# Optimization experiments

Measured on AMD Instinct MI355X. Metric: run time of the kernel, lower is better.

## Reference

```python
import jax, jax.numpy as jnp
import numpy as np

B, S, E = 256, 512, 768          # batch, seq_len, embed_dim (= 2*hidden_dim)
MD = 2 * 384 + 1                 # memory feature dim after location column = 769
HOPS, OUT = 3, 3


def setup_inputs() -> dict:
    key = jax.random.key(0)
    ks = jax.random.split(key, 9)
    memory = jax.random.normal(ks[0], (B, S, E), dtype=jnp.float32)
    aspect = jax.random.normal(ks[1], (B, E), dtype=jnp.float32)
    att_w = jax.random.normal(ks[2], (MD + 2 * E,), dtype=jnp.float32) * 0.02
    att_b = jnp.zeros((1,), dtype=jnp.float32)
    gru_w_ih = jax.random.normal(ks[3], (3 * E, MD), dtype=jnp.float32) * 0.02
    gru_w_hh = jax.random.normal(ks[4], (3 * E, E), dtype=jnp.float32) * 0.02
    gru_b_ih = jnp.zeros((3 * E,), dtype=jnp.float32)
    gru_b_hh = jnp.zeros((3 * E,), dtype=jnp.float32)
    dense_w = jax.random.normal(ks[5], (E, OUT), dtype=jnp.float32) * 0.02
    dense_b = jnp.zeros((OUT,), dtype=jnp.float32)
    memory_len = jax.random.randint(ks[6], (B,), S // 2, S + 1, dtype=jnp.int32)
    left_len = jax.random.randint(ks[7], (B,), 0, 64, dtype=jnp.int32)
    aspect_len = jax.random.randint(ks[8], (B,), 1, 8, dtype=jnp.int32)
    return dict(memory=memory, aspect=aspect, att_w=att_w, att_b=att_b,
                gru_w_ih=gru_w_ih, gru_w_hh=gru_w_hh, gru_b_ih=gru_b_ih,
                gru_b_hh=gru_b_hh, dense_w=dense_w, dense_b=dense_b,
                memory_len=memory_len, left_len=left_len, aspect_len=aspect_len,
                hops=HOPS)


def _locationed_memory(memory, memory_len, left_len, aspect_len):
    # Vectorized form of the nested python loop: per-position location-decay
    # weight and signed-offset column u, only for idx < memory_len.
    dt = memory.dtype
    idx = jnp.arange(memory.shape[1], dtype=jnp.int32)[None, :]   # [1,S]
    start = left_len[:, None]
    alen = aspect_len[:, None]
    mlen = memory_len[:, None]
    before = idx < start
    after_off = idx - start - alen + 1
    u = jnp.where(before, idx - start,
                  jnp.where(idx < start + alen, 0, after_off)).astype(dt)
    l = jnp.where(before, start - idx,
                  jnp.where(idx < start + alen, 0, after_off)).astype(dt)
    valid = idx < mlen
    w = jnp.where(valid, 1.0 - l / mlen.astype(dt), 1.0)
    u = jnp.where(valid, u, 0.0)
    mem = memory * w[:, :, None]
    return jnp.concatenate([mem, u[:, :, None]], axis=-1)        # [B,S,MD]


def _gru_cell(x, h, w_ih, w_hh, b_ih, b_hh):
    gi = x @ w_ih.T + b_ih
    gh = h @ w_hh.T + b_hh
    ir, iz, in_ = jnp.split(gi, 3, axis=-1)
    hr, hz, hn = jnp.split(gh, 3, axis=-1)
    r = jax.nn.sigmoid(ir + hr)
    z = jax.nn.sigmoid(iz + hz)
    n = jnp.tanh(in_ + r * hn)
    return (1.0 - z) * n + z * h


def reference(memory, aspect, att_w, att_b, gru_w_ih, gru_w_hh, gru_b_ih,
              gru_b_hh, dense_w, dense_b, memory_len, left_len, aspect_len,
              hops):
    mem = _locationed_memory(memory, memory_len, left_len, aspect_len)
    # att_linear(cat([mem, et, aspect])) split into three small matvecs
    w_mem = att_w[:MD]
    w_et = att_w[MD:MD + E]
    w_asp = att_w[MD + E:]
    g_static = mem @ w_mem + (aspect @ w_asp)[:, None] + att_b[0]  # [B,S]
    et = jnp.zeros_like(aspect)
    for _ in range(hops):
        g = g_static + (et @ w_et)[:, None]                        # [B,S]
        alpha = jax.nn.softmax(g, axis=1)
        i = jnp.einsum('bs,bsd->bd', alpha, mem)                   # [B,MD]
        et = _gru_cell(i, et, gru_w_ih, gru_w_hh, gru_b_ih, gru_b_hh)
    logits = et @ dense_w + dense_b                                # [B,OUT]
    return logits
```

## Files before the change

kernel.cpp:

```cpp
#include <hip/hip_runtime.h>
#include <math.h>

#define Bn 256
#define Sn 512
#define En 768
#define G3n 2304

typedef __attribute__((ext_vector_type(8))) short short8;
typedef __attribute__((ext_vector_type(4))) float f32x4;

__device__ __forceinline__ float sigmoidf_(float x) { return 1.f / (1.f + __expf(-x)); }
__device__ __forceinline__ float tanhf_(float x) {
  float e = __expf(2.f * x);
  return (e - 1.f) / (e + 1.f);
}

__device__ __forceinline__ unsigned short f2bf(float x) {
  unsigned int u = __builtin_bit_cast(unsigned int, x);
  u += 0x7FFFu + ((u >> 16) & 1u);
  return (unsigned short)(u >> 16);
}
__device__ __forceinline__ float bf2f(unsigned short u) {
  unsigned int x = ((unsigned int)u) << 16;
  return __builtin_bit_cast(float, x);
}

__device__ __forceinline__ void loc_uw(int s, int start, int al, int ml, float& u, float& w) {
  float uu;
  if (s < start)            uu = (float)(s - start);
  else if (s < start + al)  uu = 0.f;
  else                      uu = (float)(s - start - al + 1);
  float l = fabsf(uu);
  if (s < ml) { w = 1.f - l / (float)ml; u = uu; }
  else        { w = 1.f; u = 0.f; }
}

__global__ __launch_bounds__(1024) void k_mega(
    const float* __restrict__ mem, const float* __restrict__ att_w,
    const int* __restrict__ mlen, const int* __restrict__ llen, const int* __restrict__ alen,
    const float* __restrict__ w_ih, const float* __restrict__ w_hh,
    float* __restrict__ pacc, float* __restrict__ pm,
    float* __restrict__ pz, float* __restrict__ piu,
    unsigned short* __restrict__ wi_bf, unsigned short* __restrict__ wh_bf) {
  __shared__ float accL[16][En];
  __shared__ float mL[16], zL[16], iuL[16];
  int bc = blockIdx.x;
  int tid = threadIdx.x;

  if (bc >= 512) {
    int cb = bc - 512;
    int mat = cb >= 216;
    int t = (cb - mat * 216) * 1024 + tid;
    int idx = t * 8;
    int r = idx / En, c = idx - r * En;
    const float* src;
    unsigned short* dst;
    if (mat == 0) { src = w_ih + (size_t)r * 769 + c; dst = wi_bf + idx; }
    else          { src = w_hh + (size_t)r * En  + c; dst = wh_bf + idx; }
    unsigned int p[4];
#pragma unroll
    for (int j = 0; j < 4; ++j) {
      unsigned int lo = f2bf(src[2 * j]);
      unsigned int hi = f2bf(src[2 * j + 1]);
      p[j] = lo | (hi << 16);
    }
    *reinterpret_cast<uint4*>(dst) = make_uint4(p[0], p[1], p[2], p[3]);
    return;
  }

  int b = bc >> 1, half = bc & 1;
  int wv = tid >> 6, lane = tid & 63;

  float4 w0 = *reinterpret_cast<const float4*>(att_w + lane * 4);
  float4 w1 = *reinterpret_cast<const float4*>(att_w + 256 + lane * 4);
  float4 w2 = *reinterpret_cast<const float4*>(att_w + 512 + lane * 4);
  float wtail = att_w[En];
  int start = llen[b], al = alen[b], ml = mlen[b];
  int s0row = half * 256 + wv * 16;
  const float* base = mem + ((size_t)b * Sn + s0row) * En;

  float m = -1e30f, z = 0.f, iu = 0.f;
  float4 a0 = {0, 0, 0, 0}, a1 = {0, 0, 0, 0}, a2 = {0, 0, 0, 0};
  float4 v0 = *reinterpret_cast<const float4*>(base + lane * 4);
  float4 v1 = *reinterpret_cast<const float4*>(base + 256 + lane * 4);
  float4 v2 = *reinterpret_cast<const float4*>(base + 512 + lane * 4);

  for (int r = 0; r < 16; ++r) {
    float4 c0 = v0, c1 = v1, c2 = v2;
    if (r < 15) {
      const float* nrow = base + (size_t)(r + 1) * En;
      v0 = *reinterpret_cast<const float4*>(nrow + lane * 4);
      v1 = *reinterpret_cast<const float4*>(nrow + 256 + lane * 4);
      v2 = *reinterpret_cast<const float4*>(nrow + 512 + lane * 4);
    }
    float dot = c0.x * w0.x + c0.y * w0.y + c0.z * w0.z + c0.w * w0.w
              + c1.x * w1.x + c1.y * w1.y + c1.z * w1.z + c1.w * w1.w
              + c2.x * w2.x + c2.y * w2.y + c2.z * w2.z + c2.w * w2.w;
#pragma unroll
    for (int off = 32; off; off >>= 1) dot += __shfl_xor(dot, off);
    int s = s0row + r;
    float u, w;
    loc_uw(s, start, al, ml, u, w);
    float g = w * dot + u * wtail;
    if (g > m) {
      float f = __expf(m - g);
      z *= f; iu *= f;
      a0.x *= f; a0.y *= f; a0.z *= f; a0.w *= f;
      a1.x *= f; a1.y *= f; a1.z *= f; a1.w *= f;
      a2.x *= f; a2.y *= f; a2.z *= f; a2.w *= f;
      m = g;
    }
    float e = __expf(g - m);
    z += e; iu += e * u;
    float sc = e * w;
    a0.x += sc * c0.x; a0.y += sc * c0.y; a0.z += sc * c0.z; a0.w += sc * c0.w;
    a1.x += sc * c1.x; a1.y += sc * c1.y; a1.z += sc * c1.z; a1.w += sc * c1.w;
    a2.x += sc * c2.x; a2.y += sc * c2.y; a2.z += sc * c2.z; a2.w += sc * c2.w;
  }

  *reinterpret_cast<float4*>(&accL[wv][lane * 4])       = a0;
  *reinterpret_cast<float4*>(&accL[wv][256 + lane * 4]) = a1;
  *reinterpret_cast<float4*>(&accL[wv][512 + lane * 4]) = a2;
  if (lane == 0) { mL[wv] = m; zL[wv] = z; iuL[wv] = iu; }
  __syncthreads();

  float M = mL[0];
#pragma unroll
  for (int i = 1; i < 16; ++i) M = fmaxf(M, mL[i]);
  float f[16], Z = 0.f, IU = 0.f;
#pragma unroll
  for (int i = 0; i < 16; ++i) {
    f[i] = __expf(mL[i] - M);
    Z += zL[i] * f[i];
    IU += iuL[i] * f[i];
  }
  if (tid < En) {
    float s = 0.f;
#pragma unroll
    for (int i = 0; i < 16; ++i) s += f[i] * accL[i][tid];
    pacc[(size_t)bc * En + tid] = s;
  }
  if (tid == 0) { pm[bc] = M; pz[bc] = Z; piu[bc] = IU; }
}

__global__ __launch_bounds__(256) void k_comb(
    const float* __restrict__ pacc, const float* __restrict__ pm,
    const float* __restrict__ pz, const float* __restrict__ piu,
    unsigned short* __restrict__ ivec_bf, float* __restrict__ ivtail,
    const float* __restrict__ db, float* __restrict__ out) {
  int b = blockIdx.x, tid = threadIdx.x;
  if (b == 0) {
#pragma unroll
    for (int j = 0; j < 3; ++j) {
      int i = tid + j * 256;
      out[i] = db[i % 3];
    }
  }
  float m0 = pm[2 * b], m1 = pm[2 * b + 1];
  float M = fmaxf(m0, m1);
  float f0 = __expf(m0 - M), f1 = __expf(m1 - M);
  float Z = pz[2 * b] * f0 + pz[2 * b + 1] * f1;
  float inv = 1.f / Z;
#pragma unroll
  for (int j = 0; j < 3; ++j) {
    int d = tid + j * 256;
    float s = f0 * pacc[(size_t)(2 * b) * En + d] + f1 * pacc[(size_t)(2 * b + 1) * En + d];
    ivec_bf[(size_t)b * En + d] = f2bf(s * inv);
  }
  if (tid == 0) ivtail[b] = (piu[2 * b] * f0 + piu[2 * b + 1] * f1) * inv;
}

template <int MODE>
__global__ __launch_bounds__(256) void k_fused(
    const unsigned short* __restrict__ Abf, const unsigned short* __restrict__ Wbf,
    const float* __restrict__ ivtail, const float* __restrict__ w_ih,
    const float* __restrict__ b_ih, const float* __restrict__ b_hh,
    float* __restrict__ gi, unsigned short* __restrict__ et_out_bf,
    const float* __restrict__ dw, float* __restrict__ out) {
  __shared__ unsigned short As[32][136];
  __shared__ unsigned short Bs[3][32][136];
  int e0 = blockIdx.x * 32, m0 = blockIdx.y * 32;
  int tid = threadIdx.x;
  int lane = tid & 63, wv = tid >> 6;
  int wm = wv >> 1, we = wv & 1;
  int l15 = lane & 15, l4 = lane >> 4;

  f32x4 acc[3];
#pragma unroll
  for (int g = 0; g < 3; ++g) { acc[g][0] = 0.f; acc[g][1] = 0.f; acc[g][2] = 0.f; acc[g][3] = 0.f; }

  for (int k0 = 0; k0 < En; k0 += 128) {
    __syncthreads();
#pragma unroll
    for (int i = 0; i < 2; ++i) {
      int idx = tid + i * 256;
      int row = idx >> 4, ch = idx & 15;
      *reinterpret_cast<uint4*>(&As[row][ch * 8]) =
          *reinterpret_cast<const uint4*>(Abf + (size_t)(m0 + row) * En + k0 + ch * 8);
    }
#pragma unroll
    for (int i = 0; i < 6; ++i) {
      int idx = tid + i * 256;
      int row = idx >> 4, ch = idx & 15;
      int g = row >> 5, er = row & 31;
      *reinterpret_cast<uint4*>(&Bs[g][er][ch * 8]) =
          *reinterpret_cast<const uint4*>(Wbf + (size_t)(g * En + e0 + er) * En + k0 + ch * 8);
    }
    __syncthreads();
#pragma unroll
    for (int ks = 0; ks < 4; ++ks) {
      short8 a = *reinterpret_cast<const short8*>(&As[wm * 16 + l15][ks * 32 + l4 * 8]);
#pragma unroll
      for (int g = 0; g < 3; ++g) {
        short8 bfr = *reinterpret_cast<const short8*>(&Bs[g][we * 16 + l15][ks * 32 + l4 * 8]);
        acc[g] = __builtin_amdgcn_mfma_f32_16x16x32_bf16(a, bfr, acc[g], 0, 0, 0);
      }
    }
  }

  int ecol = e0 + we * 16 + l15;
  int mbase = m0 + wm * 16 + l4 * 4;
  float bhr = b_hh[ecol], bhz = b_hh[En + ecol], bhn = b_hh[2 * En + ecol];
  float vout[4];
  if (MODE == 0) {
    float wn0 = w_ih[(size_t)ecol * 769 + En];
    float wn1 = w_ih[(size_t)(En + ecol) * 769 + En];
    float wn2 = w_ih[(size_t)(2 * En + ecol) * 769 + En];
    float bi0 = b_ih[ecol], bi1 = b_ih[En + ecol], bi2 = b_ih[2 * En + ecol];
#pragma unroll
    for (int j = 0; j < 4; ++j) {
      int m = mbase + j;
      float au = ivtail[m];
      float gr = acc[0][j] + au * wn0 + bi0;
      float gz = acc[1][j] + au * wn1 + bi1;
      float gn = acc[2][j] + au * wn2 + bi2;
      gi[(size_t)m * G3n + ecol]          = gr;
      gi[(size_t)m * G3n + En + ecol]     = gz;
      gi[(size_t)m * G3n + 2 * En + ecol] = gn;
      float r = sigmoidf_(gr + bhr);
      float z = sigmoidf_(gz + bhz);
      float n = tanhf_(gn + r * bhn);
      vout[j] = (1.f - z) * n;
    }
  } else {
#pragma unroll
    for (int j = 0; j < 4; ++j) {
      int m = mbase + j;
      float rr = sigmoidf_(gi[(size_t)m * G3n + ecol] + acc[0][j] + bhr);
      float zz = sigmoidf_(gi[(size_t)m * G3n + En + ecol] + acc[1][j] + bhz);
      float nn = tanhf_(gi[(size_t)m * G3n + 2 * En + ecol] + rr * (acc[2][j] + bhn));
      float h = bf2f(Abf[(size_t)m * En + ecol]);
      vout[j] = (1.f - zz) * nn + zz * h;
    }
  }

  if (MODE != 2) {
#pragma unroll
    for (int j = 0; j < 4; ++j)
      et_out_bf[(size_t)(mbase + j) * En + ecol] = f2bf(vout[j]);
  } else {
    float dw0 = dw[ecol * 3 + 0], dw1 = dw[ecol * 3 + 1], dw2 = dw[ecol * 3 + 2];
    float p[4][3];
#pragma unroll
    for (int j = 0; j < 4; ++j) {
      p[j][0] = vout[j] * dw0;
      p[j][1] = vout[j] * dw1;
      p[j][2] = vout[j] * dw2;
    }
#pragma unroll
    for (int off = 1; off < 16; off <<= 1)
#pragma unroll
      for (int j = 0; j < 4; ++j) {
        p[j][0] += __shfl_xor(p[j][0], off);
        p[j][1] += __shfl_xor(p[j][1], off);
        p[j][2] += __shfl_xor(p[j][2], off);
      }
    if (l15 == 0) {
#pragma unroll
      for (int j = 0; j < 4; ++j) {
        atomicAdd(&out[(mbase + j) * 3 + 0], p[j][0]);
        atomicAdd(&out[(mbase + j) * 3 + 1], p[j][1]);
        atomicAdd(&out[(mbase + j) * 3 + 2], p[j][2]);
      }
    }
  }
}

extern "C" void kernel_launch(void* const* d_in, const int* in_sizes, int n_in,
                              void* d_out, int out_size, void* d_ws, size_t ws_size,
                              hipStream_t stream) {
  const float* memory   = (const float*)d_in[0];
  const float* att_w    = (const float*)d_in[2];
  const float* gru_w_ih = (const float*)d_in[4];
  const float* gru_w_hh = (const float*)d_in[5];
  const float* gru_b_ih = (const float*)d_in[6];
  const float* gru_b_hh = (const float*)d_in[7];
  const float* dense_w  = (const float*)d_in[8];
  const float* dense_b  = (const float*)d_in[9];
  const int* memory_len = (const int*)d_in[10];
  const int* left_len   = (const int*)d_in[11];
  const int* aspect_len = (const int*)d_in[12];
  float* out = (float*)d_out;

  unsigned short* wi_bf   = (unsigned short*)d_ws;
  unsigned short* wh_bf   = wi_bf + (size_t)G3n * En;
  unsigned short* ivec_bf = wh_bf + (size_t)G3n * En;
  unsigned short* eta_bf  = ivec_bf + (size_t)Bn * En;
  unsigned short* etb_bf  = eta_bf + (size_t)Bn * En;
  float* ivtail = (float*)(etb_bf + (size_t)Bn * En);
  float* pm     = ivtail + Bn;
  float* pz     = pm + 2 * Bn;
  float* piu    = pz + 2 * Bn;
  float* pacc   = piu + 2 * Bn;
  float* gi     = pacc + (size_t)2 * Bn * En;

  k_mega<<<dim3(944), 1024, 0, stream>>>(memory, att_w, memory_len, left_len, aspect_len,
                                         gru_w_ih, gru_w_hh, pacc, pm, pz, piu, wi_bf, wh_bf);
  k_comb<<<dim3(Bn), 256, 0, stream>>>(pacc, pm, pz, piu, ivec_bf, ivtail, dense_b, out);
  k_fused<0><<<dim3(En / 32, Bn / 32), 256, 0, stream>>>(
      ivec_bf, wi_bf, ivtail, gru_w_ih, gru_b_ih, gru_b_hh, gi, eta_bf, nullptr, nullptr);
  k_fused<1><<<dim3(En / 32, Bn / 32), 256, 0, stream>>>(
      eta_bf, wh_bf, nullptr, nullptr, nullptr, gru_b_hh, gi, etb_bf, nullptr, nullptr);
  k_fused<2><<<dim3(En / 32, Bn / 32), 256, 0, stream>>>(
      etb_bf, wh_bf, nullptr, nullptr, nullptr, gru_b_hh, gi, nullptr, dense_w, out);
}
```

Measured before the change: 120.0 us.

## Fuse softmax partial combine into first GRU GEMM and drop LDS staging

Removes the k_comb kernel. The first hop GEMM now reads the two fp32 partial accumulators directly, rescales them and converts to bf16 while forming the A fragment. It also recomputes the location-tail scalar in the epilogue. All three GEMM kernels drop shared-memory tiling and load A and B fragments straight from global memory into MFMA operands. The output-bias initialisation moves into the MODE 1 kernel. This saves one launch and the ivec round trip, but the first kernel reads twice the A data in fp32, and the lack of LDS reuse means redundant global loads of weight rows across waves.

```diff
diff --git a/kernel.cpp b/kernel.cpp
--- a/kernel.cpp
+++ b/kernel.cpp
@@ -143,42 +143,16 @@
   if (tid == 0) { pm[bc] = M; pz[bc] = Z; piu[bc] = IU; }
 }
 
-__global__ __launch_bounds__(256) void k_comb(
+template <int MODE>
+__global__ __launch_bounds__(256) void k_hop(
     const float* __restrict__ pacc, const float* __restrict__ pm,
     const float* __restrict__ pz, const float* __restrict__ piu,
-    unsigned short* __restrict__ ivec_bf, float* __restrict__ ivtail,
-    const float* __restrict__ db, float* __restrict__ out) {
-  int b = blockIdx.x, tid = threadIdx.x;
-  if (b == 0) {
-#pragma unroll
-    for (int j = 0; j < 3; ++j) {
-      int i = tid + j * 256;
-      out[i] = db[i % 3];
-    }
-  }
-  float m0 = pm[2 * b], m1 = pm[2 * b + 1];
-  float M = fmaxf(m0, m1);
-  float f0 = __expf(m0 - M), f1 = __expf(m1 - M);
-  float Z = pz[2 * b] * f0 + pz[2 * b + 1] * f1;
-  float inv = 1.f / Z;
-#pragma unroll
-  for (int j = 0; j < 3; ++j) {
-    int d = tid + j * 256;
-    float s = f0 * pacc[(size_t)(2 * b) * En + d] + f1 * pacc[(size_t)(2 * b + 1) * En + d];
-    ivec_bf[(size_t)b * En + d] = f2bf(s * inv);
-  }
-  if (tid == 0) ivtail[b] = (piu[2 * b] * f0 + piu[2 * b + 1] * f1) * inv;
-}
-
-template <int MODE>
-__global__ __launch_bounds__(256) void k_fused(
     const unsigned short* __restrict__ Abf, const unsigned short* __restrict__ Wbf,
-    const float* __restrict__ ivtail, const float* __restrict__ w_ih,
-    const float* __restrict__ b_ih, const float* __restrict__ b_hh,
-    float* __restrict__ gi, unsigned short* __restrict__ et_out_bf,
-    const float* __restrict__ dw, float* __restrict__ out) {
-  __shared__ unsigned short As[32][136];
-  __shared__ unsigned short Bs[3][32][136];
+    const float* __restrict__ w_ih, const float* __restrict__ b_ih,
+    const float* __restrict__ b_hh, float* __restrict__ gi,
+    unsigned short* __restrict__ et_out_bf,
+    const float* __restrict__ dw, const float* __restrict__ db,
+    float* __restrict__ out) {
   int e0 = blockIdx.x * 32, m0 = blockIdx.y * 32;
   int tid = threadIdx.x;
   int lane = tid & 63, wv = tid >> 6;
@@ -189,33 +163,52 @@
 #pragma unroll
   for (int g = 0; g < 3; ++g) { acc[g][0] = 0.f; acc[g][1] = 0.f; acc[g][2] = 0.f; acc[g][3] = 0.f; }
 
-  for (int k0 = 0; k0 < En; k0 += 128) {
-    __syncthreads();
-#pragma unroll
-    for (int i = 0; i < 2; ++i) {
-      int idx = tid + i * 256;
-      int row = idx >> 4, ch = idx & 15;
-      *reinterpret_cast<uint4*>(&As[row][ch * 8]) =
-          *reinterpret_cast<const uint4*>(Abf + (size_t)(m0 + row) * En + k0 + ch * 8);
-    }
-#pragma unroll
-    for (int i = 0; i < 6; ++i) {
-      int idx = tid + i * 256;
-      int row = idx >> 4, ch = idx & 15;
-      int g = row >> 5, er = row & 31;
-      *reinterpret_cast<uint4*>(&Bs[g][er][ch * 8]) =
-          *reinterpret_cast<const uint4*>(Wbf + (size_t)(g * En + e0 + er) * En + k0 + ch * 8);
-    }
-    __syncthreads();
-#pragma unroll
-    for (int ks = 0; ks < 4; ++ks) {
-      short8 a = *reinterpret_cast<const short8*>(&As[wm * 16 + l15][ks * 32 + l4 * 8]);
-#pragma unroll
-      for (int g = 0; g < 3; ++g) {
-        short8 bfr = *reinterpret_cast<const short8*>(&Bs[g][we * 16 + l15][ks * 32 + l4 * 8]);
-        acc[g] = __builtin_amdgcn_mfma_f32_16x16x32_bf16(a, bfr, acc[g], 0, 0, 0);
-      }
-    }
+  int arow = m0 + wm * 16 + l15;
+  int brow = e0 + we * 16 + l15;
+  const unsigned short* B0 = Wbf + ((size_t)(0 * En + brow)) * En + l4 * 8;
+  const unsigned short* B1 = Wbf + ((size_t)(1 * En + brow)) * En + l4 * 8;
+  const unsigned short* B2 = Wbf + ((size_t)(2 * En + brow)) * En + l4 * 8;
+
+  float f0 = 0.f, f1 = 0.f, inv = 0.f;
+  const float* p0 = nullptr;
+  const float* p1 = nullptr;
+  const unsigned short* Ap = nullptr;
+  if (MODE == 0) {
+    float ma = pm[2 * arow], mb = pm[2 * arow + 1];
+    float M = fmaxf(ma, mb);
+    f0 = __expf(ma - M); f1 = __expf(mb - M);
+    inv = 1.f / (pz[2 * arow] * f0 + pz[2 * arow + 1] * f1);
+    p0 = pacc + (size_t)(2 * arow) * En + l4 * 8;
+    p1 = p0 + En;
+  } else {
+    Ap = Abf + (size_t)arow * En + l4 * 8;
+  }
+
+#pragma unroll
+  for (int k0 = 0; k0 < En; k0 += 32) {
+    short8 a;
+    if (MODE == 0) {
+      float4 x0 = *reinterpret_cast<const float4*>(p0 + k0);
+      float4 x1 = *reinterpret_cast<const float4*>(p0 + k0 + 4);
+      float4 y0 = *reinterpret_cast<const float4*>(p1 + k0);
+      float4 y1 = *reinterpret_cast<const float4*>(p1 + k0 + 4);
+      a[0] = (short)f2bf((f0 * x0.x + f1 * y0.x) * inv);
+      a[1] = (short)f2bf((f0 * x0.y + f1 * y0.y) * inv);
+      a[2] = (short)f2bf((f0 * x0.z + f1 * y0.z) * inv);
+      a[3] = (short)f2bf((f0 * x0.w + f1 * y0.w) * inv);
+      a[4] = (short)f2bf((f0 * x1.x + f1 * y1.x) * inv);
+      a[5] = (short)f2bf((f0 * x1.y + f1 * y1.y) * inv);
+      a[6] = (short)f2bf((f0 * x1.z + f1 * y1.z) * inv);
+      a[7] = (short)f2bf((f0 * x1.w + f1 * y1.w) * inv);
+    } else {
+      a = *reinterpret_cast<const short8*>(Ap + k0);
+    }
+    short8 br = *reinterpret_cast<const short8*>(B0 + k0);
+    short8 bz = *reinterpret_cast<const short8*>(B1 + k0);
+    short8 bn = *reinterpret_cast<const short8*>(B2 + k0);
+    acc[0] = __builtin_amdgcn_mfma_f32_16x16x32_bf16(a, br, acc[0], 0, 0, 0);
+    acc[1] = __builtin_amdgcn_mfma_f32_16x16x32_bf16(a, bz, acc[1], 0, 0, 0);
+    acc[2] = __builtin_amdgcn_mfma_f32_16x16x32_bf16(a, bn, acc[2], 0, 0, 0);
   }
 
   int ecol = e0 + we * 16 + l15;
@@ -230,7 +223,11 @@
 #pragma unroll
     for (int j = 0; j < 4; ++j) {
       int m = mbase + j;
-      float au = ivtail[m];
+      float ma = pm[2 * m], mb = pm[2 * m + 1];
+      float M = fmaxf(ma, mb);
+      float g0 = __expf(ma - M), g1 = __expf(mb - M);
+      float iv = 1.f / (pz[2 * m] * g0 + pz[2 * m + 1] * g1);
+      float au = (piu[2 * m] * g0 + piu[2 * m + 1] * g1) * iv;
       float gr = acc[0][j] + au * wn0 + bi0;
       float gz = acc[1][j] + au * wn1 + bi1;
       float gn = acc[2][j] + au * wn2 + bi2;
@@ -258,6 +255,8 @@
 #pragma unroll
     for (int j = 0; j < 4; ++j)
       et_out_bf[(size_t)(mbase + j) * En + ecol] = f2bf(vout[j]);
+    if (MODE == 1 && blockIdx.x == 0 && tid < 96)
+      out[m0 * 3 + tid] = db[tid % 3];
   } else {
     float dw0 = dw[ecol * 3 + 0], dw1 = dw[ecol * 3 + 1], dw2 = dw[ecol * 3 + 2];
     float p[4][3];
@@ -304,11 +303,9 @@
 
   unsigned short* wi_bf   = (unsigned short*)d_ws;
   unsigned short* wh_bf   = wi_bf + (size_t)G3n * En;
-  unsigned short* ivec_bf = wh_bf + (size_t)G3n * En;
-  unsigned short* eta_bf  = ivec_bf + (size_t)Bn * En;
+  unsigned short* eta_bf  = wh_bf + (size_t)G3n * En;
   unsigned short* etb_bf  = eta_bf + (size_t)Bn * En;
-  float* ivtail = (float*)(etb_bf + (size_t)Bn * En);
-  float* pm     = ivtail + Bn;
+  float* pm     = (float*)(etb_bf + (size_t)Bn * En);
   float* pz     = pm + 2 * Bn;
   float* piu    = pz + 2 * Bn;
   float* pacc   = piu + 2 * Bn;
@@ -316,11 +313,13 @@
 
   k_mega<<<dim3(944), 1024, 0, stream>>>(memory, att_w, memory_len, left_len, aspect_len,
                                          gru_w_ih, gru_w_hh, pacc, pm, pz, piu, wi_bf, wh_bf);
-  k_comb<<<dim3(Bn), 256, 0, stream>>>(pacc, pm, pz, piu, ivec_bf, ivtail, dense_b, out);
-  k_fused<0><<<dim3(En / 32, Bn / 32), 256, 0, stream>>>(
-      ivec_bf, wi_bf, ivtail, gru_w_ih, gru_b_ih, gru_b_hh, gi, eta_bf, nullptr, nullptr);
-  k_fused<1><<<dim3(En / 32, Bn / 32), 256, 0, stream>>>(
-      eta_bf, wh_bf, nullptr, nullptr, nullptr, gru_b_hh, gi, etb_bf, nullptr, nullptr);
-  k_fused<2><<<dim3(En / 32, Bn / 32), 256, 0, stream>>>(
-      etb_bf, wh_bf, nullptr, nullptr, nullptr, gru_b_hh, gi, nullptr, dense_w, out);
-}
+  k_hop<0><<<dim3(En / 32, Bn / 32), 256, 0, stream>>>(
+      pacc, pm, pz, piu, nullptr, wi_bf, gru_w_ih, gru_b_ih, gru_b_hh, gi, eta_bf,
+      nullptr, nullptr, nullptr);
+  k_hop<1><<<dim3(En / 32, Bn / 32), 256, 0, stream>>>(
+      nullptr, nullptr, nullptr, nullptr, eta_bf, wh_bf, nullptr, nullptr, gru_b_hh, gi, etb_bf,
+      nullptr, dense_b, out);
+  k_hop<2><<<dim3(En / 32, Bn / 32), 256, 0, stream>>>(
+      nullptr, nullptr, nullptr, nullptr, etb_bf, wh_bf, nullptr, nullptr, gru_b_hh, gi, nullptr,
+      dense_w, nullptr, out);
+}
```

After: 140.6 us. 1.17x slower.

## Split K across two wave groups in GRU GEMM kernels with LDS reduction

Applied to the files above, without the earlier changes.

Each k_fused block now runs 512 threads. Two groups of four waves each handle half of every 256-wide K chunk, and the two partial accumulators are summed through shared memory before the epilogue. The aim is more waves per block and fewer K-loop iterations with barriers (3 instead of 6) for these small GEMMs, which launch only 192 blocks. The cost is more LDS per block, an extra reduction barrier, and the second wave group sitting idle during the epilogue.

```diff
diff --git a/kernel.cpp b/kernel.cpp
--- a/kernel.cpp
+++ b/kernel.cpp
@@ -171,52 +171,70 @@
 }
 
 template <int MODE>
-__global__ __launch_bounds__(256) void k_fused(
+__global__ __launch_bounds__(512) void k_fused(
     const unsigned short* __restrict__ Abf, const unsigned short* __restrict__ Wbf,
     const float* __restrict__ ivtail, const float* __restrict__ w_ih,
     const float* __restrict__ b_ih, const float* __restrict__ b_hh,
     float* __restrict__ gi, unsigned short* __restrict__ et_out_bf,
-    const float* __restrict__ dw, float* __restrict__ out) {
-  __shared__ unsigned short As[32][136];
-  __shared__ unsigned short Bs[3][32][136];
+    const float* __restrict__ dw, const float* __restrict__ db,
+    float* __restrict__ out) {
+  __shared__ unsigned short As[32][264];
+  __shared__ unsigned short Bs[3][32][264];
+  __shared__ float red[4][64][17];
   int e0 = blockIdx.x * 32, m0 = blockIdx.y * 32;
   int tid = threadIdx.x;
   int lane = tid & 63, wv = tid >> 6;
-  int wm = wv >> 1, we = wv & 1;
+  int p = wv & 3, kh = wv >> 2;
+  int wm = p >> 1, we = p & 1;
   int l15 = lane & 15, l4 = lane >> 4;
 
   f32x4 acc[3];
 #pragma unroll
   for (int g = 0; g < 3; ++g) { acc[g][0] = 0.f; acc[g][1] = 0.f; acc[g][2] = 0.f; acc[g][3] = 0.f; }
 
-  for (int k0 = 0; k0 < En; k0 += 128) {
+  for (int kb = 0; kb < 3; ++kb) {
+    int kbase = kb * 256;
     __syncthreads();
 #pragma unroll
     for (int i = 0; i < 2; ++i) {
-      int idx = tid + i * 256;
-      int row = idx >> 4, ch = idx & 15;
+      int idx = tid + i * 512;
+      int row = idx >> 5, ch = idx & 31;
       *reinterpret_cast<uint4*>(&As[row][ch * 8]) =
-          *reinterpret_cast<const uint4*>(Abf + (size_t)(m0 + row) * En + k0 + ch * 8);
+          *reinterpret_cast<const uint4*>(Abf + (size_t)(m0 + row) * En + kbase + ch * 8);
     }
 #pragma unroll
     for (int i = 0; i < 6; ++i) {
-      int idx = tid + i * 256;
-      int row = idx >> 4, ch = idx & 15;
-      int g = row >> 5, er = row & 31;
-      *reinterpret_cast<uint4*>(&Bs[g][er][ch * 8]) =
-          *reinterpret_cast<const uint4*>(Wbf + (size_t)(g * En + e0 + er) * En + k0 + ch * 8);
+      int idx = tid + i * 512;
+      int g = idx >> 10, rem = idx & 1023;
+      int row = rem >> 5, ch = rem & 31;
+      *reinterpret_cast<uint4*>(&Bs[g][row][ch * 8]) =
+          *reinterpret_cast<const uint4*>(Wbf + (size_t)(g * En + e0 + row) * En + kbase + ch * 8);
     }
     __syncthreads();
 #pragma unroll
     for (int ks = 0; ks < 4; ++ks) {
-      short8 a = *reinterpret_cast<const short8*>(&As[wm * 16 + l15][ks * 32 + l4 * 8]);
+      int col = kh * 128 + ks * 32 + l4 * 8;
+      short8 a = *reinterpret_cast<const short8*>(&As[wm * 16 + l15][col]);
 #pragma unroll
       for (int g = 0; g < 3; ++g) {
-        short8 bfr = *reinterpret_cast<const short8*>(&Bs[g][we * 16 + l15][ks * 32 + l4 * 8]);
+        short8 bfr = *reinterpret_cast<const short8*>(&Bs[g][we * 16 + l15][col]);
         acc[g] = __builtin_amdgcn_mfma_f32_16x16x32_bf16(a, bfr, acc[g], 0, 0, 0);
       }
     }
   }
+
+  if (kh == 1) {
+#pragma unroll
+    for (int g = 0; g < 3; ++g)
+#pragma unroll
+      for (int j = 0; j < 4; ++j) red[p][lane][g * 4 + j] = acc[g][j];
+  }
+  __syncthreads();
+  if (kh == 1) return;
+#pragma unroll
+  for (int g = 0; g < 3; ++g)
+#pragma unroll
+    for (int j = 0; j < 4; ++j) acc[g][j] += red[p][lane][g * 4 + j];
 
   int ecol = e0 + we * 16 + l15;
   int mbase = m0 + wm * 16 + l4 * 4;
@@ -260,27 +278,27 @@
       et_out_bf[(size_t)(mbase + j) * En + ecol] = f2bf(vout[j]);
   } else {
     float dw0 = dw[ecol * 3 + 0], dw1 = dw[ecol * 3 + 1], dw2 = dw[ecol * 3 + 2];
-    float p[4][3];
+    float pp[4][3];
 #pragma unroll
     for (int j = 0; j < 4; ++j) {
-      p[j][0] = vout[j] * dw0;
-      p[j][1] = vout[j] * dw1;
-      p[j][2] = vout[j] * dw2;
+      pp[j][0] = vout[j] * dw0;
+      pp[j][1] = vout[j] * dw1;
+      pp[j][2] = vout[j] * dw2;
     }
 #pragma unroll
     for (int off = 1; off < 16; off <<= 1)
 #pragma unroll
       for (int j = 0; j < 4; ++j) {
-        p[j][0] += __shfl_xor(p[j][0], off);
-        p[j][1] += __shfl_xor(p[j][1], off);
-        p[j][2] += __shfl_xor(p[j][2], off);
+        pp[j][0] += __shfl_xor(pp[j][0], off);
+        pp[j][1] += __shfl_xor(pp[j][1], off);
+        pp[j][2] += __shfl_xor(pp[j][2], off);
       }
     if (l15 == 0) {
 #pragma unroll
       for (int j = 0; j < 4; ++j) {
-        atomicAdd(&out[(mbase + j) * 3 + 0], p[j][0]);
-        atomicAdd(&out[(mbase + j) * 3 + 1], p[j][1]);
-        atomicAdd(&out[(mbase + j) * 3 + 2], p[j][2]);
+        atomicAdd(&out[(mbase + j) * 3 + 0], pp[j][0]);
+        atomicAdd(&out[(mbase + j) * 3 + 1], pp[j][1]);
+        atomicAdd(&out[(mbase + j) * 3 + 2], pp[j][2]);
       }
     }
   }
@@ -317,10 +335,10 @@
   k_mega<<<dim3(944), 1024, 0, stream>>>(memory, att_w, memory_len, left_len, aspect_len,
                                          gru_w_ih, gru_w_hh, pacc, pm, pz, piu, wi_bf, wh_bf);
   k_comb<<<dim3(Bn), 256, 0, stream>>>(pacc, pm, pz, piu, ivec_bf, ivtail, dense_b, out);
-  k_fused<0><<<dim3(En / 32, Bn / 32), 256, 0, stream>>>(
-      ivec_bf, wi_bf, ivtail, gru_w_ih, gru_b_ih, gru_b_hh, gi, eta_bf, nullptr, nullptr);
-  k_fused<1><<<dim3(En / 32, Bn / 32), 256, 0, stream>>>(
-      eta_bf, wh_bf, nullptr, nullptr, nullptr, gru_b_hh, gi, etb_bf, nullptr, nullptr);
-  k_fused<2><<<dim3(En / 32, Bn / 32), 256, 0, stream>>>(
-      etb_bf, wh_bf, nullptr, nullptr, nullptr, gru_b_hh, gi, nullptr, dense_w, out);
-}
+  k_fused<0><<<dim3(En / 32, Bn / 32), 512, 0, stream>>>(
+      ivec_bf, wi_bf, ivtail, gru_w_ih, gru_b_ih, gru_b_hh, gi, eta_bf, nullptr, nullptr, nullptr);
+  k_fused<1><<<dim3(En / 32, Bn / 32), 512, 0, stream>>>(
+      eta_bf, wh_bf, nullptr, nullptr, nullptr, gru_b_hh, gi, etb_bf, nullptr, nullptr, nullptr);
+  k_fused<2><<<dim3(En / 32, Bn / 32), 512, 0, stream>>>(
+      etb_bf, wh_bf, nullptr, nullptr, nullptr, gru_b_hh, gi, nullptr, dense_w, nullptr, out);
+}
```

New measurement: 116.7 us. 2.7% less time.
